# Optimization experiments

Hardware: AMD Instinct MI355X
Metric: run time of the kernel (lower is better)

Reference implementation:

```python
import math
import jax, jax.numpy as jnp
import numpy as np

N = 64
N_CP = 16

# Chirp phase exp(j*pi*k^2/N), computed in float64 (as in torch) then cast to complex64.
_k = np.arange(N, dtype=np.float64)
CHIRP = np.exp(1j * np.pi * _k ** 2 / N).astype(np.complex64)  # [N]


def setup_inputs() -> dict:
    key = jax.random.key(0)
    k1, k2 = jax.random.split(key)
    batch, num_sym = 256, 512
    symbols_real = jax.random.normal(k1, (batch, num_sym, N), dtype=jnp.float32)
    symbols_imag = jax.random.normal(k2, (batch, num_sym, N), dtype=jnp.float32)
    return {"symbols_real": symbols_real, "symbols_imag": symbols_imag}


def reference(symbols_real, symbols_imag):
    # [batch, num_sym, N] complex64
    symbols = jax.lax.complex(symbols_real, symbols_imag)
    chirp = jnp.asarray(CHIRP)
    chirped = symbols * chirp                          # pre-chirp multiply
    td = jnp.fft.ifft(chirped, n=N, axis=-1) * math.sqrt(N)  # DFnT time domain
    cp = td[..., -N_CP:]                               # cyclic prefix
    td_cp = jnp.concatenate([cp, td], axis=-1)         # [batch, num_sym, N+N_cp]
    batch = symbols.shape[0]
    signal = td_cp.reshape(batch, -1)                  # [batch, num_sym*(N+N_cp)]
    # complex output returned as stacked (real, imag) float32
    return jnp.stack([signal.real, signal.imag], axis=-1).astype(jnp.float32)
```

## Files before the change

### kernel.cpp

```cpp
#include <hip/hip_runtime.h>


__global__ __launch_bounds__(256) void ocdm_kernel(
    const float* __restrict__ sym_re,
    const float* __restrict__ sym_im,
    float2* __restrict__ out,
    int n_rows)
{
    const int l = threadIdx.x & 63;
    const int w = threadIdx.x >> 6;
    const int wave_global = blockIdx.x * (blockDim.x >> 6) + w;
    const int wave_stride = gridDim.x * (blockDim.x >> 6);

    __shared__ float2 lds[4][64];

    float cr, ci;
    {
        float f = (float)((l * l) & 127) * (1.0f / 64.0f);
        cr = 0.125f * cospif(f);
        ci = 0.125f * sinpif(f);
    }

    const int D[6] = {32, 16, 8, 4, 2, 1};
    float twr[6], twi[6], sg[6];
#pragma unroll
    for (int s = 0; s < 6; ++s) {
        int d = D[s];
        int j = l & (d - 1);
        bool up = (l & d) != 0;
        float f = (float)j / (float)d;
        twr[s] = up ? cospif(f) : 1.0f;
        twi[s] = up ? sinpif(f) : 0.0f;
        sg[s]  = up ? -1.0f : 1.0f;
    }

    const int n = (int)(__brev((unsigned)l) >> 26);

    for (int r = wave_global; r < n_rows; r += wave_stride) {
        const int idx = r * 64 + l;
        float srr = sym_re[idx];
        float sii = sym_im[idx];
        float xr = srr * cr - sii * ci;
        float xi = srr * ci + sii * cr;

#pragma unroll
        for (int s = 0; s < 6; ++s) {
            float pr = __shfl_xor(xr, D[s]);
            float pi = __shfl_xor(xi, D[s]);
            float ar = fmaf(sg[s], xr, pr);
            float ai = fmaf(sg[s], xi, pi);
            float nr = ar * twr[s] - ai * twi[s];
            float ni = fmaf(ar, twi[s], ai * twr[s]);
            xr = nr;
            xi = ni;
        }

        lds[w][n] = make_float2(xr, xi);
        asm volatile("s_waitcnt lgkmcnt(0)" ::: "memory");
        float2 v = lds[w][(l + 48) & 63];

        const long ob = (long)r * 80;
        out[ob + l] = v;
        if (l < 16)
            out[ob + 64 + l] = v;
    }
}

extern "C" void kernel_launch(void* const* d_in, const int* in_sizes, int n_in,
                              void* d_out, int out_size, void* d_ws, size_t ws_size,
                              hipStream_t stream) {
    const float* sym_re = (const float*)d_in[0];
    const float* sym_im = (const float*)d_in[1];
    float2* out = (float2*)d_out;

    const int n_rows = in_sizes[0] / 64;

    int blocks = (n_rows + 3) / 4;
    if (blocks > 2048) blocks = 2048;
    ocdm_kernel<<<blocks, 256, 0, stream>>>(sym_re, sym_im, out, n_rows);
}
```

Before: 35.27 us.

## Process four rows per wave with float4 loads and radix-4 FFT split

Each wave now handles four 64-point rows at once. Each lane loads four consecutive samples through float4 loads, runs four radix-2 shuffle stages across 16 lanes, then finishes with an in-register radix-4 butterfly. The cyclic-prefix output is assembled in LDS and written as five coalesced float2 stores per lane. The goal is fewer shuffles per point and wider memory transactions, at the cost of more registers and a larger LDS buffer. It assumes the row count is a multiple of four.

```diff
diff --git a/kernel.cpp b/kernel.cpp
--- a/kernel.cpp
+++ b/kernel.cpp
@@ -2,80 +2,123 @@
 
 
 __global__ __launch_bounds__(256) void ocdm_kernel(
-    const float* __restrict__ sym_re,
-    const float* __restrict__ sym_im,
+    const float4* __restrict__ re4,
+    const float4* __restrict__ im4,
     float2* __restrict__ out,
-    int n_rows)
+    int n_groups)
 {
     const int l = threadIdx.x & 63;
     const int w = threadIdx.x >> 6;
+    const int g = l >> 4;
+    const int j = l & 15;
     const int wave_global = blockIdx.x * (blockDim.x >> 6) + w;
     const int wave_stride = gridDim.x * (blockDim.x >> 6);
 
-    __shared__ float2 lds[4][64];
+    __shared__ float2 lds[4][320];
 
-    float cr, ci;
-    {
-        float f = (float)((l * l) & 127) * (1.0f / 64.0f);
-        cr = 0.125f * cospif(f);
-        ci = 0.125f * sinpif(f);
+    float ckr[4], cki[4];
+#pragma unroll
+    for (int q = 0; q < 4; ++q) {
+        int k = 4 * j + q;
+        float f = (float)((k * k) & 127) * (1.0f / 64.0f);
+        ckr[q] = 0.125f * cospif(f);
+        cki[q] = 0.125f * sinpif(f);
     }
 
-    const int D[6] = {32, 16, 8, 4, 2, 1};
-    float twr[6], twi[6], sg[6];
+    const int D[4] = {8, 4, 2, 1};
+    float twr[4], twi[4], sg[4];
 #pragma unroll
-    for (int s = 0; s < 6; ++s) {
+    for (int s = 0; s < 4; ++s) {
         int d = D[s];
-        int j = l & (d - 1);
-        bool up = (l & d) != 0;
-        float f = (float)j / (float)d;
+        int jj = j & (d - 1);
+        bool up = (j & d) != 0;
+        float f = (float)jj / (float)d;
         twr[s] = up ? cospif(f) : 1.0f;
         twi[s] = up ? sinpif(f) : 0.0f;
         sg[s]  = up ? -1.0f : 1.0f;
     }
 
-    const int n = (int)(__brev((unsigned)l) >> 26);
+    const int m = (int)(__brev((unsigned)j) >> 28);
 
-    for (int r = wave_global; r < n_rows; r += wave_stride) {
-        const int idx = r * 64 + l;
-        float srr = sym_re[idx];
-        float sii = sym_im[idx];
-        float xr = srr * cr - sii * ci;
-        float xi = srr * ci + sii * cr;
+    float tqr[3], tqi[3];
+#pragma unroll
+    for (int q = 1; q <= 3; ++q) {
+        float f = (float)(m * q) * (1.0f / 32.0f);
+        tqr[q - 1] = cospif(f);
+        tqi[q - 1] = sinpif(f);
+    }
+
+    const int wbase = g * 80;
+
+    for (int r = wave_global; r < n_groups; r += wave_stride) {
+        float4 vr = re4[r * 64 + l];
+        float4 vi = im4[r * 64 + l];
+
+        float xr[4], xi[4];
+        {
+            const float rr[4] = {vr.x, vr.y, vr.z, vr.w};
+            const float ii[4] = {vi.x, vi.y, vi.z, vi.w};
+#pragma unroll
+            for (int q = 0; q < 4; ++q) {
+                xr[q] = rr[q] * ckr[q] - ii[q] * cki[q];
+                xi[q] = fmaf(rr[q], cki[q], ii[q] * ckr[q]);
+            }
+        }
 
 #pragma unroll
-        for (int s = 0; s < 6; ++s) {
-            float pr = __shfl_xor(xr, D[s]);
-            float pi = __shfl_xor(xi, D[s]);
-            float ar = fmaf(sg[s], xr, pr);
-            float ai = fmaf(sg[s], xi, pi);
-            float nr = ar * twr[s] - ai * twi[s];
-            float ni = fmaf(ar, twi[s], ai * twr[s]);
-            xr = nr;
-            xi = ni;
+        for (int s = 0; s < 4; ++s) {
+#pragma unroll
+            for (int q = 0; q < 4; ++q) {
+                float pr = __shfl_xor(xr[q], D[s]);
+                float pi = __shfl_xor(xi[q], D[s]);
+                float ar = fmaf(sg[s], xr[q], pr);
+                float ai = fmaf(sg[s], xi[q], pi);
+                xr[q] = ar * twr[s] - ai * twi[s];
+                xi[q] = fmaf(ar, twi[s], ai * twr[s]);
+            }
         }
 
-        lds[w][n] = make_float2(xr, xi);
+#pragma unroll
+        for (int q = 1; q <= 3; ++q) {
+            float ar = xr[q] * tqr[q - 1] - xi[q] * tqi[q - 1];
+            float ai = fmaf(xr[q], tqi[q - 1], xi[q] * tqr[q - 1]);
+            xr[q] = ar; xi[q] = ai;
+        }
+
+        float Ar = xr[0] + xr[2], Ai = xi[0] + xi[2];
+        float Br = xr[0] - xr[2], Bi = xi[0] - xi[2];
+        float Cr = xr[1] + xr[3], Ci = xi[1] + xi[3];
+        float Dr = xr[1] - xr[3], Di = xi[1] - xi[3];
+        float2 X0 = make_float2(Ar + Cr, Ai + Ci);
+        float2 X1 = make_float2(Br - Di, Bi + Dr);
+        float2 X2 = make_float2(Ar - Cr, Ai - Ci);
+        float2 X3 = make_float2(Br + Di, Bi - Dr);
+
+        lds[w][wbase + m + 16] = X0;
+        lds[w][wbase + m + 32] = X1;
+        lds[w][wbase + m + 48] = X2;
+        lds[w][wbase + m]      = X3;
+        lds[w][wbase + m + 64] = X3;
         asm volatile("s_waitcnt lgkmcnt(0)" ::: "memory");
-        float2 v = lds[w][(l + 48) & 63];
 
-        const long ob = (long)r * 80;
-        out[ob + l] = v;
-        if (l < 16)
-            out[ob + 64 + l] = v;
+        const long ob = (long)r * 320;
+#pragma unroll
+        for (int i = 0; i < 5; ++i)
+            out[ob + i * 64 + l] = lds[w][i * 64 + l];
     }
 }
 
 extern "C" void kernel_launch(void* const* d_in, const int* in_sizes, int n_in,
                               void* d_out, int out_size, void* d_ws, size_t ws_size,
                               hipStream_t stream) {
-    const float* sym_re = (const float*)d_in[0];
-    const float* sym_im = (const float*)d_in[1];
+    const float4* re4 = (const float4*)d_in[0];
+    const float4* im4 = (const float4*)d_in[1];
     float2* out = (float2*)d_out;
 
     const int n_rows = in_sizes[0] / 64;
+    const int n_groups = n_rows / 4;
 
-    int blocks = (n_rows + 3) / 4;
+    int blocks = (n_groups + 3) / 4;
     if (blocks > 2048) blocks = 2048;
-    ocdm_kernel<<<blocks, 256, 0, stream>>>(sym_re, sym_im, out, n_rows);
+    ocdm_kernel<<<blocks, 256, 0, stream>>>(re4, im4, out, n_groups);
 }
```

Measured after the change: 30.97 us. 12.2% less time.
